# Kernel optimization log

Measured on AMD Instinct MI355X. Metric: run time of the kernel, lower is better.

The kernel has to match this reference:

```python
import jax, jax.numpy as jnp
from jax import lax
import numpy as np

E = 16          # n_routed_experts
H = 2048        # hidden_size
I = 1408        # moe_intermediate_size
T = 2048        # tokens
K = 6           # top_k


def setup_inputs() -> dict:
    key = jax.random.key(0)
    k1, k2, k3, k4, k5 = jax.random.split(key, 5)
    hidden_states = jax.random.normal(k1, (T, H), dtype=jnp.float32)
    top_k_index = jax.random.randint(k2, (T, K), 0, E)
    top_k_weights = jax.random.uniform(k3, (T, K), dtype=jnp.float32)
    gate_up_proj = jax.random.normal(k4, (E, 2 * I, H), dtype=jnp.float32) * 0.02
    down_proj = jax.random.normal(k5, (E, H, I), dtype=jnp.float32) * 0.02
    return {
        "hidden_states": hidden_states,
        "top_k_index": top_k_index,
        "top_k_weights": top_k_weights,
        "gate_up_proj": gate_up_proj,
        "down_proj": down_proj,
    }


def reference(hidden_states, top_k_index, top_k_weights, gate_up_proj, down_proj):
    # combine[t, e] = sum over k-slots of top_k_weights[t, k] where top_k_index[t, k] == e
    # (scatter-add handles duplicate expert picks identically to index_add_).
    n_tok = hidden_states.shape[0]
    n_exp = gate_up_proj.shape[0]
    combine = jnp.zeros((n_tok, n_exp), hidden_states.dtype)
    combine = combine.at[jnp.arange(n_tok)[:, None], top_k_index].add(top_k_weights)

    def expert_step(acc, params):
        gu, dn, c_e = params  # gu: [2I, H], dn: [H, I], c_e: [n_tok]
        gate, up = jnp.split(hidden_states @ gu.T, 2, axis=-1)  # each [n_tok, I]
        y = (jax.nn.silu(gate) * up) @ dn.T                     # [n_tok, H]
        return acc + y * c_e[:, None], None

    out, _ = lax.scan(
        expert_step,
        jnp.zeros_like(hidden_states),
        (gate_up_proj, down_proj, combine.T),
    )
    return out
```

## Files before the change

kernel.cpp:

```cpp
#include <hip/hip_runtime.h>
#include <hip/hip_bf16.h>
#include <cstdint>

#define T_TOK 2048
#define HD 2048
#define ID 1408
#define NE 16
#define TOPK 6

#define BM 256
#define BN 64
#define BK 64

typedef __bf16 bf16x8 __attribute__((ext_vector_type(8)));
typedef float f32x4 __attribute__((ext_vector_type(4)));

typedef const __attribute__((address_space(1))) void* gas1_t;
typedef __attribute__((address_space(3))) void* las3_t;
#define GLDS16(g, l) __builtin_amdgcn_global_load_lds((gas1_t)(g), (las3_t)(l), 16, 0, 0)


__global__ void k_combine(const int* __restrict__ idx, const float* __restrict__ w,
                          float* __restrict__ combine) {
    int t = blockIdx.x * blockDim.x + threadIdx.x;
    if (t >= T_TOK) return;
    int ie[TOPK];
    float fw[TOPK];
#pragma unroll
    for (int k = 0; k < TOPK; k++) { ie[k] = idx[t * TOPK + k]; fw[k] = w[t * TOPK + k]; }
#pragma unroll
    for (int e = 0; e < NE; e++) {
        float s = 0.f;
#pragma unroll
        for (int k = 0; k < TOPK; k++) if (ie[k] == e) s += fw[k];
        combine[t * NE + e] = s;
    }
}

__global__ void k_lists(const float* __restrict__ combine, int* __restrict__ counts,
                        int* __restrict__ tok, float* __restrict__ wts) {
    int t = blockIdx.x * blockDim.x + threadIdx.x;
    if (t >= T_TOK) return;
    for (int e = 0; e < NE; e++) {
        float c = combine[t * NE + e];
        if (c != 0.0f) {
            int p = atomicAdd(&counts[e], 1);
            tok[e * T_TOK + p] = t;
            wts[e * T_TOK + p] = c;
        }
    }
}

__global__ void k_cvt(const float* __restrict__ x, __bf16* __restrict__ xb) {
    int i = (blockIdx.x * 256 + threadIdx.x) * 8;
    float4 a = *(const float4*)(x + i);
    float4 b = *(const float4*)(x + i + 4);
    bf16x8 o;
    o[0] = (__bf16)a.x; o[1] = (__bf16)a.y; o[2] = (__bf16)a.z; o[3] = (__bf16)a.w;
    o[4] = (__bf16)b.x; o[5] = (__bf16)b.y; o[6] = (__bf16)b.z; o[7] = (__bf16)b.w;
    *(bf16x8*)(xb + i) = o;
}


__device__ __forceinline__ int swz(int row, int cb) {
    return row * 128 + (cb ^ ((row & 7) << 4));
}

__device__ __forceinline__ bf16x8 ldfrag(const __bf16* base, int row, int cb) {
    return *(const bf16x8*)((const char*)base + swz(row, cb));
}

__device__ __forceinline__ void stage8(const float* __restrict__ src, char* lds,
                                       int row, int cb) {
    float4 f0 = ((const float4*)src)[0];
    float4 f1 = ((const float4*)src)[1];
    bf16x8 o;
    o[0] = (__bf16)f0.x; o[1] = (__bf16)f0.y; o[2] = (__bf16)f0.z; o[3] = (__bf16)f0.w;
    o[4] = (__bf16)f1.x; o[5] = (__bf16)f1.y; o[6] = (__bf16)f1.z; o[7] = (__bf16)f1.w;
    *(bf16x8*)(lds + swz(row, cb)) = o;
}


__global__ __launch_bounds__(512, 4) void k_gemm1(
    const __bf16* __restrict__ Xb, const float* __restrict__ gup,
    const int* __restrict__ counts, const int* __restrict__ tok,
    __bf16* __restrict__ act) {
    int x = blockIdx.x;
    int e = x / 22;
    int n0 = (x % 22) * BN;
    int cnt = counts[e];
    int m0 = blockIdx.y * BM;
    if (m0 >= cnt) return;

    __shared__ __align__(16) __bf16 sA[BM * BK];
    __shared__ __align__(16) __bf16 sBg[BN * BK];
    __shared__ __align__(16) __bf16 sBu[BN * BK];

    int tid = threadIdx.x;
    int lane = tid & 63;
    int wid = tid >> 6;

    const __bf16* pA[4];
    int csw = ((lane & 7) ^ ((lane >> 3) & 7)) * 8;
#pragma unroll
    for (int j = 0; j < 4; j++) {
        int r = 32 * wid + 8 * j + (lane >> 3);
        int g = m0 + r;
        if (g >= cnt) g = cnt - 1;
        pA[j] = Xb + (size_t)tok[e * T_TOK + g] * HD + csw;
    }

    int br = tid >> 3, bc = tid & 7;
    const float* gbase = gup + (size_t)e * (2 * ID) * HD;
    const float* bgSrc = gbase + (size_t)(n0 + br) * HD + bc * 8;
    const float* buSrc = gbase + (size_t)(ID + n0 + br) * HD + bc * 8;

    int wm = wid >> 1, wn = wid & 1;
    int l15 = lane & 15, lh = lane >> 4;

    f32x4 accg[4][2] = {};
    f32x4 accu[4][2] = {};

    for (int k0 = 0; k0 < HD; k0 += BK) {
        __syncthreads();
#pragma unroll
        for (int j = 0; j < 4; j++)
            GLDS16(pA[j] + k0, &sA[(32 * wid + 8 * j) * BK]);
        stage8(bgSrc + k0, (char*)sBg, br, bc * 16);
        stage8(buSrc + k0, (char*)sBu, br, bc * 16);
        __syncthreads();
#pragma unroll
        for (int kk = 0; kk < 2; kk++) {
            int cb = kk * 64 + lh * 16;
            bf16x8 a[4];
#pragma unroll
            for (int fm = 0; fm < 4; fm++)
                a[fm] = ldfrag(sA, wm * 64 + fm * 16 + l15, cb);
#pragma unroll
            for (int fn = 0; fn < 2; fn++) {
                bf16x8 bg = ldfrag(sBg, wn * 32 + fn * 16 + l15, cb);
                bf16x8 bu = ldfrag(sBu, wn * 32 + fn * 16 + l15, cb);
#pragma unroll
                for (int fm = 0; fm < 4; fm++) {
                    accg[fm][fn] = __builtin_amdgcn_mfma_f32_16x16x32_bf16(a[fm], bg, accg[fm][fn], 0, 0, 0);
                    accu[fm][fn] = __builtin_amdgcn_mfma_f32_16x16x32_bf16(a[fm], bu, accu[fm][fn], 0, 0, 0);
                }
            }
        }
    }

#pragma unroll
    for (int fm = 0; fm < 4; fm++) {
#pragma unroll
        for (int fn = 0; fn < 2; fn++) {
#pragma unroll
            for (int j = 0; j < 4; j++) {
                int mloc = wm * 64 + fm * 16 + lh * 4 + j;
                int g = m0 + mloc;
                if (g < cnt) {
                    float gv = accg[fm][fn][j];
                    float uv = accu[fm][fn][j];
                    float sv = gv * (1.0f / (1.0f + __expf(-gv)));
                    int n = n0 + wn * 32 + fn * 16 + l15;
                    act[((size_t)e * T_TOK + g) * ID + n] = (__bf16)(sv * uv);
                }
            }
        }
    }
}


__global__ __launch_bounds__(512, 6) void k_gemm2(
    const __bf16* __restrict__ act, const float* __restrict__ dn,
    const int* __restrict__ counts, const int* __restrict__ tok,
    const float* __restrict__ wts, float* __restrict__ out) {
    int x = blockIdx.x;
    int e = x >> 5;
    int n0 = (x & 31) * BN;
    int cnt = counts[e];
    int m0 = blockIdx.y * BM;
    if (m0 >= cnt) return;

    __shared__ __align__(16) __bf16 sA[BM * BK];
    __shared__ __align__(16) __bf16 sB[BN * BK];
    __shared__ int tokLds[BM];
    __shared__ float wtLds[BM];

    int tid = threadIdx.x;
    if (tid < BM) {
        int g = m0 + tid;
        bool v = g < cnt;
        tokLds[tid] = v ? tok[e * T_TOK + g] : 0;
        wtLds[tid] = v ? wts[e * T_TOK + g] : 0.f;
    }

    int lane = tid & 63;
    int wid = tid >> 6;

    const __bf16* pA[4];
    int csw = ((lane & 7) ^ ((lane >> 3) & 7)) * 8;
#pragma unroll
    for (int j = 0; j < 4; j++) {
        int r = 32 * wid + 8 * j + (lane >> 3);
        pA[j] = act + ((size_t)e * T_TOK + m0 + r) * ID + csw;
    }

    int br = tid >> 3, bc = tid & 7;
    const float* bSrc = dn + (size_t)e * HD * ID + (size_t)(n0 + br) * ID + bc * 8;

    int wm = wid >> 1, wn = wid & 1;
    int l15 = lane & 15, lh = lane >> 4;

    f32x4 acc[4][2] = {};

    for (int k0 = 0; k0 < ID; k0 += BK) {
        __syncthreads();
#pragma unroll
        for (int j = 0; j < 4; j++)
            GLDS16(pA[j] + k0, &sA[(32 * wid + 8 * j) * BK]);
        stage8(bSrc + k0, (char*)sB, br, bc * 16);
        __syncthreads();
#pragma unroll
        for (int kk = 0; kk < 2; kk++) {
            int cb = kk * 64 + lh * 16;
            bf16x8 a[4];
#pragma unroll
            for (int fm = 0; fm < 4; fm++)
                a[fm] = ldfrag(sA, wm * 64 + fm * 16 + l15, cb);
#pragma unroll
            for (int fn = 0; fn < 2; fn++) {
                bf16x8 b = ldfrag(sB, wn * 32 + fn * 16 + l15, cb);
#pragma unroll
                for (int fm = 0; fm < 4; fm++)
                    acc[fm][fn] = __builtin_amdgcn_mfma_f32_16x16x32_bf16(a[fm], b, acc[fm][fn], 0, 0, 0);
            }
        }
    }

#pragma unroll
    for (int fm = 0; fm < 4; fm++) {
#pragma unroll
        for (int fn = 0; fn < 2; fn++) {
#pragma unroll
            for (int j = 0; j < 4; j++) {
                int mloc = wm * 64 + fm * 16 + lh * 4 + j;
                int g = m0 + mloc;
                if (g < cnt) {
                    float v = acc[fm][fn][j] * wtLds[mloc];
                    int n = n0 + wn * 32 + fn * 16 + l15;
                    atomicAdd(&out[(size_t)tokLds[mloc] * HD + n], v);
                }
            }
        }
    }
}


extern "C" void kernel_launch(void* const* d_in, const int* in_sizes, int n_in,
                              void* d_out, int out_size, void* d_ws, size_t ws_size,
                              hipStream_t stream) {
    const float* hs = (const float*)d_in[0];
    const int* tki = (const int*)d_in[1];
    const float* tkw = (const float*)d_in[2];
    const float* gup = (const float*)d_in[3];
    const float* dnp = (const float*)d_in[4];
    float* out = (float*)d_out;

    char* p = (char*)d_ws;
    int* counts = (int*)p;      p += 256;
    float* combine = (float*)p; p += (size_t)T_TOK * NE * 4;
    int* tok = (int*)p;         p += (size_t)NE * T_TOK * 4;
    float* wts = (float*)p;     p += (size_t)NE * T_TOK * 4;
    __bf16* Xb = (__bf16*)p;    p += (size_t)T_TOK * HD * 2;
    __bf16* act = (__bf16*)p;

    hipMemsetAsync(counts, 0, 256, stream);
    hipMemsetAsync(d_out, 0, (size_t)T_TOK * HD * 4, stream);
    k_combine<<<T_TOK / 256, 256, 0, stream>>>(tki, tkw, combine);
    k_lists<<<T_TOK / 256, 256, 0, stream>>>(combine, counts, tok, wts);
    k_cvt<<<(T_TOK * HD / 8) / 256, 256, 0, stream>>>(hs, Xb);
    k_gemm1<<<dim3(22 * NE, T_TOK / BM), 512, 0, stream>>>(Xb, gup, counts, tok, act);
    k_gemm2<<<dim3(32 * NE, T_TOK / BM), 512, 0, stream>>>(act, dnp, counts, tok, wts, out);
}
```

Measured before the change: 459.7 us.

## Double-buffer A tiles and register-prefetch weights in both MoE GEMM kernels

Both expert GEMM kernels now keep two LDS buffers for the gathered activation tile. The next K-step's A tile is issued with global_load_lds, and the next fp32 weight slice is loaded into registers, while MFMAs run on the current tile. This aims to hide global-memory latency behind compute, where before each iteration stalled on its loads. The cost is extra LDS per block, which lowers the number of resident blocks, plus more live registers; the gemm2 launch-bounds occupancy hint also drops from 6 to 4.

Result: slower. 471.0 us (+2.5%).

```diff
diff --git a/kernel.cpp b/kernel.cpp
--- a/kernel.cpp
+++ b/kernel.cpp
@@ -70,10 +70,7 @@
     return *(const bf16x8*)((const char*)base + swz(row, cb));
 }
 
-__device__ __forceinline__ void stage8(const float* __restrict__ src, char* lds,
-                                       int row, int cb) {
-    float4 f0 = ((const float4*)src)[0];
-    float4 f1 = ((const float4*)src)[1];
+__device__ __forceinline__ void stage8v(char* lds, int row, int cb, float4 f0, float4 f1) {
     bf16x8 o;
     o[0] = (__bf16)f0.x; o[1] = (__bf16)f0.y; o[2] = (__bf16)f0.z; o[3] = (__bf16)f0.w;
     o[4] = (__bf16)f1.x; o[5] = (__bf16)f1.y; o[6] = (__bf16)f1.z; o[7] = (__bf16)f1.w;
@@ -92,7 +89,7 @@
     int m0 = blockIdx.y * BM;
     if (m0 >= cnt) return;
 
-    __shared__ __align__(16) __bf16 sA[BM * BK];
+    __shared__ __align__(16) __bf16 sA[2][BM * BK];
     __shared__ __align__(16) __bf16 sBg[BN * BK];
     __shared__ __align__(16) __bf16 sBu[BN * BK];
 
@@ -121,21 +118,39 @@
     f32x4 accg[4][2] = {};
     f32x4 accu[4][2] = {};
 
-    for (int k0 = 0; k0 < HD; k0 += BK) {
+    float4 g0 = ((const float4*)bgSrc)[0], g1 = ((const float4*)bgSrc)[1];
+    float4 u0 = ((const float4*)buSrc)[0], u1 = ((const float4*)buSrc)[1];
+#pragma unroll
+    for (int j = 0; j < 4; j++)
+        GLDS16(pA[j], &sA[0][(32 * wid + 8 * j) * BK]);
+    __syncthreads();
+
+    const int NT = HD / BK;
+    for (int k = 0; k < NT; k++) {
+        int cur = k & 1;
+        stage8v((char*)sBg, br, bc * 16, g0, g1);
+        stage8v((char*)sBu, br, bc * 16, u0, u1);
         __syncthreads();
-#pragma unroll
-        for (int j = 0; j < 4; j++)
-            GLDS16(pA[j] + k0, &sA[(32 * wid + 8 * j) * BK]);
-        stage8(bgSrc + k0, (char*)sBg, br, bc * 16);
-        stage8(buSrc + k0, (char*)sBu, br, bc * 16);
-        __syncthreads();
+
+        if (k + 1 < NT) {
+            int k0 = (k + 1) * BK;
+#pragma unroll
+            for (int j = 0; j < 4; j++)
+                GLDS16(pA[j] + k0, &sA[cur ^ 1][(32 * wid + 8 * j) * BK]);
+            const float* bg = bgSrc + k0;
+            const float* bu = buSrc + k0;
+            g0 = ((const float4*)bg)[0]; g1 = ((const float4*)bg)[1];
+            u0 = ((const float4*)bu)[0]; u1 = ((const float4*)bu)[1];
+        }
+
+        const __bf16* sAc = sA[cur];
 #pragma unroll
         for (int kk = 0; kk < 2; kk++) {
             int cb = kk * 64 + lh * 16;
             bf16x8 a[4];
 #pragma unroll
             for (int fm = 0; fm < 4; fm++)
-                a[fm] = ldfrag(sA, wm * 64 + fm * 16 + l15, cb);
+                a[fm] = ldfrag(sAc, wm * 64 + fm * 16 + l15, cb);
 #pragma unroll
             for (int fn = 0; fn < 2; fn++) {
                 bf16x8 bg = ldfrag(sBg, wn * 32 + fn * 16 + l15, cb);
@@ -147,6 +162,7 @@
                 }
             }
         }
+        __syncthreads();
     }
 
 #pragma unroll
@@ -170,7 +186,7 @@
 }
 
 
-__global__ __launch_bounds__(512, 6) void k_gemm2(
+__global__ __launch_bounds__(512, 4) void k_gemm2(
     const __bf16* __restrict__ act, const float* __restrict__ dn,
     const int* __restrict__ counts, const int* __restrict__ tok,
     const float* __restrict__ wts, float* __restrict__ out) {
@@ -181,7 +197,7 @@
     int m0 = blockIdx.y * BM;
     if (m0 >= cnt) return;
 
-    __shared__ __align__(16) __bf16 sA[BM * BK];
+    __shared__ __align__(16) __bf16 sA[2][BM * BK];
     __shared__ __align__(16) __bf16 sB[BN * BK];
     __shared__ int tokLds[BM];
     __shared__ float wtLds[BM];
@@ -213,20 +229,35 @@
 
     f32x4 acc[4][2] = {};
 
-    for (int k0 = 0; k0 < ID; k0 += BK) {
+    float4 b0 = ((const float4*)bSrc)[0], b1 = ((const float4*)bSrc)[1];
+#pragma unroll
+    for (int j = 0; j < 4; j++)
+        GLDS16(pA[j], &sA[0][(32 * wid + 8 * j) * BK]);
+    __syncthreads();
+
+    const int NT = ID / BK;
+    for (int k = 0; k < NT; k++) {
+        int cur = k & 1;
+        stage8v((char*)sB, br, bc * 16, b0, b1);
         __syncthreads();
-#pragma unroll
-        for (int j = 0; j < 4; j++)
-            GLDS16(pA[j] + k0, &sA[(32 * wid + 8 * j) * BK]);
-        stage8(bSrc + k0, (char*)sB, br, bc * 16);
-        __syncthreads();
+
+        if (k + 1 < NT) {
+            int k0 = (k + 1) * BK;
+#pragma unroll
+            for (int j = 0; j < 4; j++)
+                GLDS16(pA[j] + k0, &sA[cur ^ 1][(32 * wid + 8 * j) * BK]);
+            const float* bs = bSrc + k0;
+            b0 = ((const float4*)bs)[0]; b1 = ((const float4*)bs)[1];
+        }
+
+        const __bf16* sAc = sA[cur];
 #pragma unroll
         for (int kk = 0; kk < 2; kk++) {
             int cb = kk * 64 + lh * 16;
             bf16x8 a[4];
 #pragma unroll
             for (int fm = 0; fm < 4; fm++)
-                a[fm] = ldfrag(sA, wm * 64 + fm * 16 + l15, cb);
+                a[fm] = ldfrag(sAc, wm * 64 + fm * 16 + l15, cb);
 #pragma unroll
             for (int fn = 0; fn < 2; fn++) {
                 bf16x8 b = ldfrag(sB, wn * 32 + fn * 16 + l15, cb);
@@ -235,6 +266,7 @@
                     acc[fm][fn] = __builtin_amdgcn_mfma_f32_16x16x32_bf16(a[fm], b, acc[fm][fn], 0, 0, 0);
             }
         }
+        __syncthreads();
     }
 
 #pragma unroll
```

## Double-buffer A tiles and register-prefetch B in both MoE GEMM kernels

Applied to the files above, without the earlier changes.

Both expert GEMM kernels now keep two LDS buffers for the activation tile, filled asynchronously with global_load_lds two k-steps ahead. The fp32 weight tile for the next step is prefetched into registers while the current step's MFMAs run. Each k-step now uses raw s_barrier and an lgkmcnt wait instead of two __syncthreads, and s_setprio raises wave priority during the MFMA block. The goal is to hide global load latency behind matrix math. In exchange the larger LDS footprint and extra live registers lower the number of resident blocks, and k_gemm2's launch bound drops from 6 to 4.

After: 900.8 us. +96.0%, slower.

```diff
diff --git a/kernel.cpp b/kernel.cpp
--- a/kernel.cpp
+++ b/kernel.cpp
@@ -18,6 +18,9 @@
 typedef const __attribute__((address_space(1))) void* gas1_t;
 typedef __attribute__((address_space(3))) void* las3_t;
 #define GLDS16(g, l) __builtin_amdgcn_global_load_lds((gas1_t)(g), (las3_t)(l), 16, 0, 0)
+
+#define BAR() do { asm volatile("" ::: "memory"); __builtin_amdgcn_s_barrier(); asm volatile("" ::: "memory"); } while (0)
+#define WAITL0 asm volatile("s_waitcnt lgkmcnt(0)" ::: "memory")
 
 
 __global__ void k_combine(const int* __restrict__ idx, const float* __restrict__ w,
@@ -70,10 +73,7 @@
     return *(const bf16x8*)((const char*)base + swz(row, cb));
 }
 
-__device__ __forceinline__ void stage8(const float* __restrict__ src, char* lds,
-                                       int row, int cb) {
-    float4 f0 = ((const float4*)src)[0];
-    float4 f1 = ((const float4*)src)[1];
+__device__ __forceinline__ void stage8v(char* lds, int row, int cb, float4 f0, float4 f1) {
     bf16x8 o;
     o[0] = (__bf16)f0.x; o[1] = (__bf16)f0.y; o[2] = (__bf16)f0.z; o[3] = (__bf16)f0.w;
     o[4] = (__bf16)f1.x; o[5] = (__bf16)f1.y; o[6] = (__bf16)f1.z; o[7] = (__bf16)f1.w;
@@ -92,7 +92,7 @@
     int m0 = blockIdx.y * BM;
     if (m0 >= cnt) return;
 
-    __shared__ __align__(16) __bf16 sA[BM * BK];
+    __shared__ __align__(16) __bf16 sA[2][BM * BK];
     __shared__ __align__(16) __bf16 sBg[BN * BK];
     __shared__ __align__(16) __bf16 sBu[BN * BK];
 
@@ -121,33 +121,70 @@
     f32x4 accg[4][2] = {};
     f32x4 accu[4][2] = {};
 
-    for (int k0 = 0; k0 < HD; k0 += BK) {
-        __syncthreads();
-#pragma unroll
-        for (int j = 0; j < 4; j++)
-            GLDS16(pA[j] + k0, &sA[(32 * wid + 8 * j) * BK]);
-        stage8(bgSrc + k0, (char*)sBg, br, bc * 16);
-        stage8(buSrc + k0, (char*)sBu, br, bc * 16);
-        __syncthreads();
-#pragma unroll
-        for (int kk = 0; kk < 2; kk++) {
-            int cb = kk * 64 + lh * 16;
-            bf16x8 a[4];
-#pragma unroll
-            for (int fm = 0; fm < 4; fm++)
-                a[fm] = ldfrag(sA, wm * 64 + fm * 16 + l15, cb);
-#pragma unroll
-            for (int fn = 0; fn < 2; fn++) {
-                bf16x8 bg = ldfrag(sBg, wn * 32 + fn * 16 + l15, cb);
-                bf16x8 bu = ldfrag(sBu, wn * 32 + fn * 16 + l15, cb);
-#pragma unroll
-                for (int fm = 0; fm < 4; fm++) {
-                    accg[fm][fn] = __builtin_amdgcn_mfma_f32_16x16x32_bf16(a[fm], bg, accg[fm][fn], 0, 0, 0);
-                    accu[fm][fn] = __builtin_amdgcn_mfma_f32_16x16x32_bf16(a[fm], bu, accu[fm][fn], 0, 0, 0);
-                }
-            }
-        }
-    }
+    const int NT = HD / BK;
+
+#pragma unroll
+    for (int j = 0; j < 4; j++)
+        GLDS16(pA[j], &sA[0][(32 * wid + 8 * j) * BK]);
+    float4 g0a = ((const float4*)bgSrc)[0], g1a = ((const float4*)bgSrc)[1];
+    float4 u0a = ((const float4*)buSrc)[0], u1a = ((const float4*)buSrc)[1];
+#pragma unroll
+    for (int j = 0; j < 4; j++)
+        GLDS16(pA[j] + BK, &sA[1][(32 * wid + 8 * j) * BK]);
+    float4 g0b, g1b, u0b, u1b;
+
+#define G1_MFMA(CUR)                                                            \
+    {                                                                           \
+        const __bf16* sAc = sA[CUR];                                            \
+        __builtin_amdgcn_s_setprio(1);                                          \
+        _Pragma("unroll")                                                       \
+        for (int kk = 0; kk < 2; kk++) {                                        \
+            int cb = kk * 64 + lh * 16;                                         \
+            bf16x8 a[4];                                                        \
+            _Pragma("unroll")                                                   \
+            for (int fm = 0; fm < 4; fm++)                                      \
+                a[fm] = ldfrag(sAc, wm * 64 + fm * 16 + l15, cb);               \
+            _Pragma("unroll")                                                   \
+            for (int fn = 0; fn < 2; fn++) {                                    \
+                bf16x8 bg = ldfrag(sBg, wn * 32 + fn * 16 + l15, cb);           \
+                bf16x8 bu = ldfrag(sBu, wn * 32 + fn * 16 + l15, cb);           \
+                _Pragma("unroll")                                               \
+                for (int fm = 0; fm < 4; fm++) {                                \
+                    accg[fm][fn] = __builtin_amdgcn_mfma_f32_16x16x32_bf16(a[fm], bg, accg[fm][fn], 0, 0, 0); \
+                    accu[fm][fn] = __builtin_amdgcn_mfma_f32_16x16x32_bf16(a[fm], bu, accu[fm][fn], 0, 0, 0); \
+                }                                                               \
+            }                                                                   \
+        }                                                                       \
+        __builtin_amdgcn_s_setprio(0);                                          \
+    }
+
+#define G1_ITER(K, SG0, SG1, SU0, SU1, LG0, LG1, LU0, LU1, CUR)                 \
+    {                                                                           \
+        stage8v((char*)sBg, br, bc * 16, SG0, SG1);     \
+        stage8v((char*)sBu, br, bc * 16, SU0, SU1);                             \
+        WAITL0;                                                                 \
+        BAR();                                                                  \
+        if ((K) + 1 < NT) {                                                     \
+            const float* bg = bgSrc + ((K) + 1) * BK;                           \
+            const float* bu = buSrc + ((K) + 1) * BK;                           \
+            LG0 = ((const float4*)bg)[0]; LG1 = ((const float4*)bg)[1];         \
+            LU0 = ((const float4*)bu)[0]; LU1 = ((const float4*)bu)[1];         \
+        }                                                                       \
+        G1_MFMA(CUR);                                                           \
+        BAR();                                                                  \
+        if ((K) + 2 < NT) {                                                     \
+            _Pragma("unroll")                                                   \
+            for (int j = 0; j < 4; j++)                                         \
+                GLDS16(pA[j] + ((K) + 2) * BK, &sA[CUR][(32 * wid + 8 * j) * BK]); \
+        }                                                                       \
+    }
+
+    for (int k = 0; k < NT; k += 2) {
+        G1_ITER(k,     g0a, g1a, u0a, u1a, g0b, g1b, u0b, u1b, 0);
+        G1_ITER(k + 1, g0b, g1b, u0b, u1b, g0a, g1a, u0a, u1a, 1);
+    }
+#undef G1_ITER
+#undef G1_MFMA
 
 #pragma unroll
     for (int fm = 0; fm < 4; fm++) {
@@ -170,7 +207,7 @@
 }
 
 
-__global__ __launch_bounds__(512, 6) void k_gemm2(
+__global__ __launch_bounds__(512, 4) void k_gemm2(
     const __bf16* __restrict__ act, const float* __restrict__ dn,
     const int* __restrict__ counts, const int* __restrict__ tok,
     const float* __restrict__ wts, float* __restrict__ out) {
@@ -181,7 +218,7 @@
     int m0 = blockIdx.y * BM;
     if (m0 >= cnt) return;
 
-    __shared__ __align__(16) __bf16 sA[BM * BK];
+    __shared__ __align__(16) __bf16 sA[2][BM * BK];
     __shared__ __align__(16) __bf16 sB[BN * BK];
     __shared__ int tokLds[BM];
     __shared__ float wtLds[BM];
@@ -213,29 +250,63 @@
 
     f32x4 acc[4][2] = {};
 
-    for (int k0 = 0; k0 < ID; k0 += BK) {
-        __syncthreads();
-#pragma unroll
-        for (int j = 0; j < 4; j++)
-            GLDS16(pA[j] + k0, &sA[(32 * wid + 8 * j) * BK]);
-        stage8(bSrc + k0, (char*)sB, br, bc * 16);
-        __syncthreads();
-#pragma unroll
-        for (int kk = 0; kk < 2; kk++) {
-            int cb = kk * 64 + lh * 16;
-            bf16x8 a[4];
-#pragma unroll
-            for (int fm = 0; fm < 4; fm++)
-                a[fm] = ldfrag(sA, wm * 64 + fm * 16 + l15, cb);
-#pragma unroll
-            for (int fn = 0; fn < 2; fn++) {
-                bf16x8 b = ldfrag(sB, wn * 32 + fn * 16 + l15, cb);
-#pragma unroll
-                for (int fm = 0; fm < 4; fm++)
-                    acc[fm][fn] = __builtin_amdgcn_mfma_f32_16x16x32_bf16(a[fm], b, acc[fm][fn], 0, 0, 0);
-            }
-        }
-    }
+    const int NT = ID / BK;
+
+#pragma unroll
+    for (int j = 0; j < 4; j++)
+        GLDS16(pA[j], &sA[0][(32 * wid + 8 * j) * BK]);
+    float4 b0a = ((const float4*)bSrc)[0], b1a = ((const float4*)bSrc)[1];
+#pragma unroll
+    for (int j = 0; j < 4; j++)
+        GLDS16(pA[j] + BK, &sA[1][(32 * wid + 8 * j) * BK]);
+    float4 b0b, b1b;
+
+#define G2_MFMA(CUR)                                                            \
+    {                                                                           \
+        const __bf16* sAc = sA[CUR];                                            \
+        __builtin_amdgcn_s_setprio(1);                                          \
+        _Pragma("unroll")                                                       \
+        for (int kk = 0; kk < 2; kk++) {                                        \
+            int cb = kk * 64 + lh * 16;                                         \
+            bf16x8 a[4];                                                        \
+            _Pragma("unroll")                                                   \
+            for (int fm = 0; fm < 4; fm++)                                      \
+                a[fm] = ldfrag(sAc, wm * 64 + fm * 16 + l15, cb);               \
+            _Pragma("unroll")                                                   \
+            for (int fn = 0; fn < 2; fn++) {                                    \
+                bf16x8 b = ldfrag(sB, wn * 32 + fn * 16 + l15, cb);             \
+                _Pragma("unroll")                                               \
+                for (int fm = 0; fm < 4; fm++)                                  \
+                    acc[fm][fn] = __builtin_amdgcn_mfma_f32_16x16x32_bf16(a[fm], b, acc[fm][fn], 0, 0, 0); \
+            }                                                                   \
+        }                                                                       \
+        __builtin_amdgcn_s_setprio(0);                                          \
+    }
+
+#define G2_ITER(K, SB0, SB1, LB0, LB1, CUR)                                     \
+    {                                                                           \
+        stage8v((char*)sB, br, bc * 16, SB0, SB1);                              \
+        WAITL0;                                                                 \
+        BAR();                                                                  \
+        if ((K) + 1 < NT) {                                                     \
+            const float* bs = bSrc + ((K) + 1) * BK;                            \
+            LB0 = ((const float4*)bs)[0]; LB1 = ((const float4*)bs)[1];         \
+        }                                                                       \
+        G2_MFMA(CUR);                                                           \
+        BAR();                                                                  \
+        if ((K) + 2 < NT) {                                                     \
+            _Pragma("unroll")                                                   \
+            for (int j = 0; j < 4; j++)                                         \
+                GLDS16(pA[j] + ((K) + 2) * BK, &sA[CUR][(32 * wid + 8 * j) * BK]); \
+        }                                                                       \
+    }
+
+    for (int k = 0; k < NT; k += 2) {
+        G2_ITER(k,     b0a, b1a, b0b, b1b, 0);
+        G2_ITER(k + 1, b0b, b1b, b0a, b1a, 1);
+    }
+#undef G2_ITER
+#undef G2_MFMA
 
 #pragma unroll
     for (int fm = 0; fm < 4; fm++) {
```

## Use persistent blocks with atomic work queue for both expert GEMMs

Applied to the files above, without the earlier changes.

Replaces the fixed 2D grid, where many blocks exit immediately because their M tile lies past the expert's token count, with 768 persistent blocks. Each block pulls work items from a global atomic cursor and decodes them into (expert, m-tile, n-tile), ordered m-fastest so blocks sharing weight tiles run close together. This is meant to remove empty-block launch overhead and improve load balance and L2 reuse of the weights. In exchange it adds an atomic and an extra barrier per tile, and lowers gemm2's occupancy hint from 6 to 4.

Result: faster. 443.1 us (-3.6%).

```diff
diff --git a/kernel.cpp b/kernel.cpp
--- a/kernel.cpp
+++ b/kernel.cpp
@@ -11,6 +11,8 @@
 #define BM 256
 #define BN 64
 #define BK 64
+#define NT1 22
+#define NT2 32
 
 typedef __bf16 bf16x8 __attribute__((ext_vector_type(8)));
 typedef float f32x4 __attribute__((ext_vector_type(4)));
@@ -80,89 +82,108 @@
     *(bf16x8*)(lds + swz(row, cb)) = o;
 }
 
+__device__ __forceinline__ bool decode_item(const int* cnts, int it, int ntn,
+                                            int& e, int& m, int& n, int& cnt) {
+    int r = it;
+#pragma unroll
+    for (int ee = 0; ee < NE; ee++) {
+        int c = cnts[ee];
+        int nm = (c + BM - 1) >> 8;
+        int tot = nm * ntn;
+        if (r < tot) { e = ee; m = r % nm; n = r / nm; cnt = c; return true; }
+        r -= tot;
+    }
+    return false;
+}
+
 
 __global__ __launch_bounds__(512, 4) void k_gemm1(
     const __bf16* __restrict__ Xb, const float* __restrict__ gup,
     const int* __restrict__ counts, const int* __restrict__ tok,
-    __bf16* __restrict__ act) {
-    int x = blockIdx.x;
-    int e = x / 22;
-    int n0 = (x % 22) * BN;
-    int cnt = counts[e];
-    int m0 = blockIdx.y * BM;
-    if (m0 >= cnt) return;
-
+    __bf16* __restrict__ act, int* __restrict__ cursor) {
     __shared__ __align__(16) __bf16 sA[BM * BK];
     __shared__ __align__(16) __bf16 sBg[BN * BK];
     __shared__ __align__(16) __bf16 sBu[BN * BK];
+    __shared__ int s_it;
 
     int tid = threadIdx.x;
     int lane = tid & 63;
     int wid = tid >> 6;
-
-    const __bf16* pA[4];
-    int csw = ((lane & 7) ^ ((lane >> 3) & 7)) * 8;
-#pragma unroll
-    for (int j = 0; j < 4; j++) {
-        int r = 32 * wid + 8 * j + (lane >> 3);
-        int g = m0 + r;
-        if (g >= cnt) g = cnt - 1;
-        pA[j] = Xb + (size_t)tok[e * T_TOK + g] * HD + csw;
-    }
-
-    int br = tid >> 3, bc = tid & 7;
-    const float* gbase = gup + (size_t)e * (2 * ID) * HD;
-    const float* bgSrc = gbase + (size_t)(n0 + br) * HD + bc * 8;
-    const float* buSrc = gbase + (size_t)(ID + n0 + br) * HD + bc * 8;
-
     int wm = wid >> 1, wn = wid & 1;
     int l15 = lane & 15, lh = lane >> 4;
-
-    f32x4 accg[4][2] = {};
-    f32x4 accu[4][2] = {};
-
-    for (int k0 = 0; k0 < HD; k0 += BK) {
+    int csw = ((lane & 7) ^ ((lane >> 3) & 7)) * 8;
+    int br = tid >> 3, bc = tid & 7;
+
+    int cnts[NE];
+#pragma unroll
+    for (int ee = 0; ee < NE; ee++) cnts[ee] = counts[ee];
+
+    while (true) {
+        if (tid == 0) s_it = atomicAdd(cursor, 1);
         __syncthreads();
-#pragma unroll
-        for (int j = 0; j < 4; j++)
-            GLDS16(pA[j] + k0, &sA[(32 * wid + 8 * j) * BK]);
-        stage8(bgSrc + k0, (char*)sBg, br, bc * 16);
-        stage8(buSrc + k0, (char*)sBu, br, bc * 16);
-        __syncthreads();
-#pragma unroll
-        for (int kk = 0; kk < 2; kk++) {
-            int cb = kk * 64 + lh * 16;
-            bf16x8 a[4];
-#pragma unroll
-            for (int fm = 0; fm < 4; fm++)
-                a[fm] = ldfrag(sA, wm * 64 + fm * 16 + l15, cb);
-#pragma unroll
-            for (int fn = 0; fn < 2; fn++) {
-                bf16x8 bg = ldfrag(sBg, wn * 32 + fn * 16 + l15, cb);
-                bf16x8 bu = ldfrag(sBu, wn * 32 + fn * 16 + l15, cb);
-#pragma unroll
-                for (int fm = 0; fm < 4; fm++) {
-                    accg[fm][fn] = __builtin_amdgcn_mfma_f32_16x16x32_bf16(a[fm], bg, accg[fm][fn], 0, 0, 0);
-                    accu[fm][fn] = __builtin_amdgcn_mfma_f32_16x16x32_bf16(a[fm], bu, accu[fm][fn], 0, 0, 0);
+        int e, m, n, cnt;
+        if (!decode_item(cnts, s_it, NT1, e, m, n, cnt)) break;
+        int m0 = m * BM;
+        int n0 = n * BN;
+
+        const __bf16* pA[4];
+#pragma unroll
+        for (int j = 0; j < 4; j++) {
+            int r = 32 * wid + 8 * j + (lane >> 3);
+            int g = m0 + r;
+            if (g >= cnt) g = cnt - 1;
+            pA[j] = Xb + (size_t)tok[e * T_TOK + g] * HD + csw;
+        }
+        const float* gbase = gup + (size_t)e * (2 * ID) * HD;
+        const float* bgSrc = gbase + (size_t)(n0 + br) * HD + bc * 8;
+        const float* buSrc = gbase + (size_t)(ID + n0 + br) * HD + bc * 8;
+
+        f32x4 accg[4][2] = {};
+        f32x4 accu[4][2] = {};
+
+        for (int k0 = 0; k0 < HD; k0 += BK) {
+            __syncthreads();
+#pragma unroll
+            for (int j = 0; j < 4; j++)
+                GLDS16(pA[j] + k0, &sA[(32 * wid + 8 * j) * BK]);
+            stage8(bgSrc + k0, (char*)sBg, br, bc * 16);
+            stage8(buSrc + k0, (char*)sBu, br, bc * 16);
+            __syncthreads();
+#pragma unroll
+            for (int kk = 0; kk < 2; kk++) {
+                int cb = kk * 64 + lh * 16;
+                bf16x8 a[4];
+#pragma unroll
+                for (int fm = 0; fm < 4; fm++)
+                    a[fm] = ldfrag(sA, wm * 64 + fm * 16 + l15, cb);
+#pragma unroll
+                for (int fn = 0; fn < 2; fn++) {
+                    bf16x8 bg = ldfrag(sBg, wn * 32 + fn * 16 + l15, cb);
+                    bf16x8 bu = ldfrag(sBu, wn * 32 + fn * 16 + l15, cb);
+#pragma unroll
+                    for (int fm = 0; fm < 4; fm++) {
+                        accg[fm][fn] = __builtin_amdgcn_mfma_f32_16x16x32_bf16(a[fm], bg, accg[fm][fn], 0, 0, 0);
+                        accu[fm][fn] = __builtin_amdgcn_mfma_f32_16x16x32_bf16(a[fm], bu, accu[fm][fn], 0, 0, 0);
+                    }
                 }
             }
         }
-    }
-
-#pragma unroll
-    for (int fm = 0; fm < 4; fm++) {
-#pragma unroll
-        for (int fn = 0; fn < 2; fn++) {
-#pragma unroll
-            for (int j = 0; j < 4; j++) {
-                int mloc = wm * 64 + fm * 16 + lh * 4 + j;
-                int g = m0 + mloc;
-                if (g < cnt) {
-                    float gv = accg[fm][fn][j];
-                    float uv = accu[fm][fn][j];
-                    float sv = gv * (1.0f / (1.0f + __expf(-gv)));
-                    int n = n0 + wn * 32 + fn * 16 + l15;
-                    act[((size_t)e * T_TOK + g) * ID + n] = (__bf16)(sv * uv);
+
+#pragma unroll
+        for (int fm = 0; fm < 4; fm++) {
+#pragma unroll
+            for (int fn = 0; fn < 2; fn++) {
+#pragma unroll
+                for (int j = 0; j < 4; j++) {
+                    int mloc = wm * 64 + fm * 16 + lh * 4 + j;
+                    int g = m0 + mloc;
+                    if (g < cnt) {
+                        float gv = accg[fm][fn][j];
+                        float uv = accu[fm][fn][j];
+                        float sv = gv * (1.0f / (1.0f + __expf(-gv)));
+                        int nn = n0 + wn * 32 + fn * 16 + l15;
+                        act[((size_t)e * T_TOK + g) * ID + nn] = (__bf16)(sv * uv);
+                    }
                 }
             }
         }
@@ -170,85 +191,94 @@
 }
 
 
-__global__ __launch_bounds__(512, 6) void k_gemm2(
+__global__ __launch_bounds__(512, 4) void k_gemm2(
     const __bf16* __restrict__ act, const float* __restrict__ dn,
     const int* __restrict__ counts, const int* __restrict__ tok,
-    const float* __restrict__ wts, float* __restrict__ out) {
-    int x = blockIdx.x;
-    int e = x >> 5;
-    int n0 = (x & 31) * BN;
-    int cnt = counts[e];
-    int m0 = blockIdx.y * BM;
-    if (m0 >= cnt) return;
-
+    const float* __restrict__ wts, float* __restrict__ out,
+    int* __restrict__ cursor) {
     __shared__ __align__(16) __bf16 sA[BM * BK];
     __shared__ __align__(16) __bf16 sB[BN * BK];
     __shared__ int tokLds[BM];
     __shared__ float wtLds[BM];
+    __shared__ int s_it;
 
     int tid = threadIdx.x;
-    if (tid < BM) {
-        int g = m0 + tid;
-        bool v = g < cnt;
-        tokLds[tid] = v ? tok[e * T_TOK + g] : 0;
-        wtLds[tid] = v ? wts[e * T_TOK + g] : 0.f;
-    }
-
     int lane = tid & 63;
     int wid = tid >> 6;
-
-    const __bf16* pA[4];
-    int csw = ((lane & 7) ^ ((lane >> 3) & 7)) * 8;
-#pragma unroll
-    for (int j = 0; j < 4; j++) {
-        int r = 32 * wid + 8 * j + (lane >> 3);
-        pA[j] = act + ((size_t)e * T_TOK + m0 + r) * ID + csw;
-    }
-
-    int br = tid >> 3, bc = tid & 7;
-    const float* bSrc = dn + (size_t)e * HD * ID + (size_t)(n0 + br) * ID + bc * 8;
-
     int wm = wid >> 1, wn = wid & 1;
     int l15 = lane & 15, lh = lane >> 4;
-
-    f32x4 acc[4][2] = {};
-
-    for (int k0 = 0; k0 < ID; k0 += BK) {
+    int csw = ((lane & 7) ^ ((lane >> 3) & 7)) * 8;
+    int br = tid >> 3, bc = tid & 7;
+
+    int cnts[NE];
+#pragma unroll
+    for (int ee = 0; ee < NE; ee++) cnts[ee] = counts[ee];
+
+    while (true) {
+        if (tid == 0) s_it = atomicAdd(cursor, 1);
         __syncthreads();
-#pragma unroll
-        for (int j = 0; j < 4; j++)
-            GLDS16(pA[j] + k0, &sA[(32 * wid + 8 * j) * BK]);
-        stage8(bSrc + k0, (char*)sB, br, bc * 16);
+        int e, m, n, cnt;
+        if (!decode_item(cnts, s_it, NT2, e, m, n, cnt)) break;
+        int m0 = m * BM;
+        int n0 = n * BN;
+
+        if (tid < BM) {
+            int g = m0 + tid;
+            bool v = g < cnt;
+            tokLds[tid] = v ? tok[e * T_TOK + g] : 0;
+            wtLds[tid] = v ? wts[e * T_TOK + g] : 0.f;
+        }
+
+        const __bf16* pA[4];
+#pragma unroll
+        for (int j = 0; j < 4; j++) {
+            int r = 32 * wid + 8 * j + (lane >> 3);
+            int g = m0 + r;
+            if (g >= cnt) g = cnt - 1;
+            pA[j] = act + ((size_t)e * T_TOK + g) * ID + csw;
+        }
+        const float* bSrc = dn + (size_t)e * HD * ID + (size_t)(n0 + br) * ID + bc * 8;
+
+        f32x4 acc[4][2] = {};
+
+        for (int k0 = 0; k0 < ID; k0 += BK) {
+            __syncthreads();
+#pragma unroll
+            for (int j = 0; j < 4; j++)
+                GLDS16(pA[j] + k0, &sA[(32 * wid + 8 * j) * BK]);
+            stage8(bSrc + k0, (char*)sB, br, bc * 16);
+            __syncthreads();
+#pragma unroll
+            for (int kk = 0; kk < 2; kk++) {
+                int cb = kk * 64 + lh * 16;
+                bf16x8 a[4];
+#pragma unroll
+                for (int fm = 0; fm < 4; fm++)
+                    a[fm] = ldfrag(sA, wm * 64 + fm * 16 + l15, cb);
+#pragma unroll
+                for (int fn = 0; fn < 2; fn++) {
+                    bf16x8 b = ldfrag(sB, wn * 32 + fn * 16 + l15, cb);
+#pragma unroll
+                    for (int fm = 0; fm < 4; fm++)
+                        acc[fm][fn] = __builtin_amdgcn_mfma_f32_16x16x32_bf16(a[fm], b, acc[fm][fn], 0, 0, 0);
+                }
+            }
+        }
+
         __syncthreads();
 #pragma unroll
-        for (int kk = 0; kk < 2; kk++) {
-            int cb = kk * 64 + lh * 16;
-            bf16x8 a[4];
-#pragma unroll
-            for (int fm = 0; fm < 4; fm++)
-                a[fm] = ldfrag(sA, wm * 64 + fm * 16 + l15, cb);
+        for (int fm = 0; fm < 4; fm++) {
 #pragma unroll
             for (int fn = 0; fn < 2; fn++) {
-                bf16x8 b = ldfrag(sB, wn * 32 + fn * 16 + l15, cb);
-#pragma unroll
-                for (int fm = 0; fm < 4; fm++)
-                    acc[fm][fn] = __builtin_amdgcn_mfma_f32_16x16x32_bf16(a[fm], b, acc[fm][fn], 0, 0, 0);
-            }
-        }
-    }
-
-#pragma unroll
-    for (int fm = 0; fm < 4; fm++) {
-#pragma unroll
-        for (int fn = 0; fn < 2; fn++) {
-#pragma unroll
-            for (int j = 0; j < 4; j++) {
-                int mloc = wm * 64 + fm * 16 + lh * 4 + j;
-                int g = m0 + mloc;
-                if (g < cnt) {
-                    float v = acc[fm][fn][j] * wtLds[mloc];
-                    int n = n0 + wn * 32 + fn * 16 + l15;
-                    atomicAdd(&out[(size_t)tokLds[mloc] * HD + n], v);
+#pragma unroll
+                for (int j = 0; j < 4; j++) {
+                    int mloc = wm * 64 + fm * 16 + lh * 4 + j;
+                    int g = m0 + mloc;
+                    if (g < cnt) {
+                        float v = acc[fm][fn][j] * wtLds[mloc];
+                        int nn = n0 + wn * 32 + fn * 16 + l15;
+                        atomicAdd(&out[(size_t)tokLds[mloc] * HD + nn], v);
+                    }
                 }
             }
         }
@@ -268,17 +298,18 @@
 
     char* p = (char*)d_ws;
     int* counts = (int*)p;      p += 256;
+    int* cursors = (int*)p;     p += 256;
     float* combine = (float*)p; p += (size_t)T_TOK * NE * 4;
     int* tok = (int*)p;         p += (size_t)NE * T_TOK * 4;
     float* wts = (float*)p;     p += (size_t)NE * T_TOK * 4;
     __bf16* Xb = (__bf16*)p;    p += (size_t)T_TOK * HD * 2;
     __bf16* act = (__bf16*)p;
 
-    hipMemsetAsync(counts, 0, 256, stream);
+    hipMemsetAsync(counts, 0, 512, stream);
     hipMemsetAsync(d_out, 0, (size_t)T_TOK * HD * 4, stream);
     k_combine<<<T_TOK / 256, 256, 0, stream>>>(tki, tkw, combine);
     k_lists<<<T_TOK / 256, 256, 0, stream>>>(combine, counts, tok, wts);
     k_cvt<<<(T_TOK * HD / 8) / 256, 256, 0, stream>>>(hs, Xb);
-    k_gemm1<<<dim3(22 * NE, T_TOK / BM), 512, 0, stream>>>(Xb, gup, counts, tok, act);
-    k_gemm2<<<dim3(32 * NE, T_TOK / BM), 512, 0, stream>>>(act, dnp, counts, tok, wts, out);
-}
+    k_gemm1<<<dim3(768), 512, 0, stream>>>(Xb, gup, counts, tok, act, &cursors[0]);
+    k_gemm2<<<dim3(768), 512, 0, stream>>>(act, dnp, counts, tok, wts, out, &cursors[1]);
+}
```
